# Kernel tuning notes

Hardware: AMD Instinct MI355X
Metric: run time of the kernel (lower is better)

## Reference

```python
import jax, jax.numpy as jnp
import numpy as np

M = 41
RHO = 4.0
HDIM = 10
NMODES = 2
BATCH = 16384


def triplet_index(m_size, rho):
    # reduced PBC triplet index set: n >= m, |m|,|n|,|m+n| <= (M-1)/2, |m*n| <= rho*(M-1)/2
    h = (m_size - 1) // 2
    idx = [(m, n) for m in range(-h, h + 1) for n in range(m, h + 1)
           if abs(m + n) <= h and abs(m * n) <= rho * h]
    return np.array(idx, dtype=np.int32)

IDX = triplet_index(M, RHO)
S = len(IDX)


def _c(a):
    # last-dim-2 real tensor -> complex
    return jax.lax.complex(a[..., 0], a[..., 1])


def setup_inputs() -> dict:
    key = jax.random.key(0)
    ks = jax.random.split(key, 6)
    x = jax.random.normal(ks[0], (BATCH, M, NMODES, 2), dtype=jnp.float32)
    task_info = jax.random.uniform(ks[1], (BATCH, 4), dtype=jnp.float32)  # col 0 = power in dBm
    pbc_C = 0.01 * jax.random.normal(ks[2], (S, 2), dtype=jnp.float32)  # complex PBC coeffs
    W1 = jax.random.normal(ks[3], (HDIM, NMODES, S, 2), dtype=jnp.float32) / np.sqrt(2.0 * NMODES * S)
    b1 = jnp.zeros((HDIM, 2), dtype=jnp.float32)
    W2 = jax.random.normal(ks[4], (HDIM, NMODES, M, 2), dtype=jnp.float32) / np.sqrt(2.0 * NMODES * M)
    b2 = jnp.zeros((HDIM, 2), dtype=jnp.float32)
    m_idx = jnp.asarray(IDX[:, 0], dtype=jnp.int32)
    n_idx = jnp.asarray(IDX[:, 1], dtype=jnp.int32)
    return {"x": x, "task_info": task_info, "pbc_C": pbc_C,
            "W1": W1, "b1": b1, "W2": W2, "b2": b2,
            "m_idx": m_idx, "n_idx": n_idx}


def _nonlinear_features(E, m_idx, n_idx):
    # E: [B, M, 2] complex -> [B, 2, S]; Manakov dual-pol triplets:
    # F[p] = (E[c+m,p]*conj(E[c+m+n,p]) + E[c+m,q]*conj(E[c+m+n,q])) * E[c+n,p]
    c = E.shape[1] // 2
    A = E[:, c + m_idx, :] * jnp.conj(E[:, c + m_idx + n_idx, :])  # [B, S, 2]
    F = (A + A[..., ::-1]) * E[:, c + n_idx, :]                    # [B, S, 2]
    return jnp.transpose(F, (0, 2, 1))                             # [B, 2, S]


def _conv_full(Wc, bc, inp):
    # ComplexConv1d whose kernel spans the whole input length (output length 1) -> [B, out]
    return jnp.einsum('oik,bik->bo', Wc, inp) + bc


def _forward(x, task_info, pbc_C, W1, b1, W2, b2, m_idx, n_idx):
    E = _c(x)                                    # [B, M, 2] complex64
    c = M // 2
    P = 10.0 ** (task_info[:, 0] / 10.0) / NMODES  # [B] launch power per mode
    F = _nonlinear_features(E, m_idx, n_idx)     # [B, 2, S]
    # EqAMPBC: center symbol + P * (triplet features . complex coeffs)
    pbc_out = E[:, c, :] + P[:, None] * jnp.einsum('bps,s->bp', F, _c(pbc_C))  # [B, 2]
    w1, bb1, w2, bb2 = _c(W1), _c(b1), _c(W2), _c(b2)
    # A = cat([f1(fo), f1(fo with pols flipped)], dim=-1) -> [B, hdim, 2]
    A = jnp.stack([_conv_full(w1, bb1, F), _conv_full(w1, bb1, F[:, ::-1, :])], axis=-1)
    Et = jnp.transpose(E, (0, 2, 1))             # [B, 2, M]
    Bm = jnp.stack([_conv_full(w2, bb2, Et), _conv_full(w2, bb2, Et[:, ::-1, :])], axis=-1)
    term = jnp.sum(A * Bm * jnp.conj(Bm) + jnp.conj(A) * Bm * Bm, axis=1)  # [B, 2]
    out = pbc_out + (1e-4 / np.sqrt(HDIM)) * term * (P[:, None] ** 2)
    return jnp.stack([out.real, out.imag], axis=-1)  # [B, 2, 2] float32


def reference(x, task_info, pbc_C, W1, b1, W2, b2, m_idx, n_idx):
    return _forward(x, task_info, pbc_C, W1, b1, W2, b2, m_idx, n_idx)
```

## Files before the change

### kernel.cpp

```cpp
#include <hip/hip_runtime.h>
#include <hip/hip_bf16.h>

typedef short bf16x8 __attribute__((ext_vector_type(8)));
typedef float f32x4  __attribute__((ext_vector_type(4)));

#define ROWS  96
#define KS1   56
#define KS2   6
#define NCOL  32

#define WP_OFF   0
#define W2P_OFF  344064

#define E_OFF    0
#define MET_OFF  10496
#define LDS_BYTES 22528

__device__ __forceinline__ unsigned short f2bf(float f) {
    union { float f; unsigned u; } v; v.f = f;
    unsigned r = v.u + 0x7FFFu + ((v.u >> 16) & 1u);
    return (unsigned short)(r >> 16);
}
__device__ __forceinline__ float bfl(unsigned u) {
    union { unsigned q; float f; } v; v.q = u << 16; return v.f;
}
__device__ __forceinline__ float bfh(unsigned u) {
    union { unsigned q; float f; } v; v.q = u & 0xffff0000u; return v.f;
}
__device__ __forceinline__ unsigned pk2(float a, float b) {
    __hip_bfloat162 h = __float22bfloat162_rn(make_float2(a, b));
    unsigned u; __builtin_memcpy(&u, &h, 4); return u;
}
__device__ __forceinline__ bf16x8 asbf(uint4 v) {
    union { uint4 u; bf16x8 b; } z; z.u = v; return z.b;
}

__global__ void prep_kernel(const float* __restrict__ W1,
                            const float* __restrict__ W2,
                            const float* __restrict__ pbcC,
                            unsigned short* __restrict__ Wp,
                            unsigned short* __restrict__ W2p, int S) {
    int idx = blockIdx.x * 256 + threadIdx.x;
    const int N1 = KS1 * ROWS * 8, N2 = KS2 * ROWS * 8;
    if (idx < N1) {
        int ks = idx / (ROWS * 8), rem = idx - ks * (ROWS * 8);
        int row = rem >> 3, kq = rem & 7;
        int s = ks * 8 + kq;
        float2 wj0 = make_float2(0.f, 0.f), wj1 = make_float2(0.f, 0.f);
        int p = 0, r = 0;
        if (s < S) {
            if (row < 80) {
                int o = row >> 2; p = (row >> 1) & 1; r = row & 1;
                wj0 = ((const float2*)W1)[(size_t)(o * 2 + 0) * S + s];
                wj1 = ((const float2*)W1)[(size_t)(o * 2 + 1) * S + s];
            } else if (row < 84) {
                p = (row >> 1) & 1; r = row & 1;
                wj0 = ((const float2*)pbcC)[s];
            }
        }
        ushort4 h; unsigned short us[4];
#pragma unroll
        for (int t = 0; t < 4; ++t) {
            int i = t & 1, cc = t >> 1, j = i ^ p;
            float2 w = j ? wj1 : wj0;
            float v = (cc == 0) ? (r ? w.y : w.x) : (r ? w.x : -w.y);
            us[t] = f2bf(v);
        }
        h.x = us[0]; h.y = us[1]; h.z = us[2]; h.w = us[3];
        ((ushort4*)Wp)[(size_t)(ks * ROWS + row) * 8 + kq] = h;
        return;
    }
    idx -= N1;
    if (idx < N2) {
        int ks = idx / (ROWS * 8), rem = idx - ks * (ROWS * 8);
        int row = rem >> 3, kq = rem & 7;
        int m = ks * 8 + kq;
        float2 wj0 = make_float2(0.f, 0.f), wj1 = make_float2(0.f, 0.f);
        int p = 0, r = 0;
        if (m < 41 && row < 80) {
            int o = row >> 2; p = (row >> 1) & 1; r = row & 1;
            wj0 = ((const float2*)W2)[(o * 2 + 0) * 41 + m];
            wj1 = ((const float2*)W2)[(o * 2 + 1) * 41 + m];
        }
        ushort4 h; unsigned short us[4];
#pragma unroll
        for (int t = 0; t < 4; ++t) {
            int i = t & 1, cc = t >> 1, j = i ^ p;
            float2 w = j ? wj1 : wj0;
            float v = (cc == 0) ? (r ? w.y : w.x) : (r ? w.x : -w.y);
            us[t] = f2bf(v);
        }
        h.x = us[0]; h.y = us[1]; h.z = us[2]; h.w = us[3];
        ((ushort4*)W2p)[(size_t)(ks * ROWS + row) * 8 + kq] = h;
    }
}

__global__ __launch_bounds__(256, 2) void eqsonn_kernel(
    const float* __restrict__ x,
    const float* __restrict__ task,
    const unsigned short* __restrict__ Wp,
    const unsigned short* __restrict__ W2p,
    const int* __restrict__ m_idx, const int* __restrict__ n_idx,
    const float* __restrict__ b1, const float* __restrict__ b2,
    float* __restrict__ out, int B, int S)
{
    __shared__ alignas(16) char ldsb[LDS_BYTES];
    const int tid  = threadIdx.x;
    const int lane = tid & 63;
    const int kh   = __builtin_amdgcn_readfirstlane(tid >> 6);
    const int l15  = lane & 15;
    const int quad = lane >> 4;
    const int b0   = blockIdx.x * NCOL;

    for (int e = tid; e < 41 * NCOL; e += 256) {
        int bb = e / 41, k = e - bb * 41;
        int bs = b0 + bb; if (bs > B - 1) bs = B - 1;
        float4 v = ((const float4*)x)[(size_t)bs * 41 + k];
        ushort4 h;
        h.x = f2bf(v.x); h.y = f2bf(v.y); h.z = f2bf(v.z); h.w = f2bf(v.w);
        *(ushort4*)(ldsb + E_OFF + (k * 16 + (bb & 15)) * 16 + (bb >> 4) * 8) = h;
    }
    for (int i = tid; i < 448; i += 256) {
        int2 mm = (i < S) ? make_int2(m_idx[i], n_idx[i]) : make_int2(0, 0);
        *(int2*)(ldsb + MET_OFF + i * 8) = mm;
    }
    __syncthreads();

    f32x4 a1[6][2], a2[5][2];
#pragma unroll
    for (int i = 0; i < 6; ++i) a1[i][0] = a1[i][1] = (f32x4){0.f,0.f,0.f,0.f};
#pragma unroll
    for (int i = 0; i < 5; ++i) a2[i][0] = a2[i][1] = (f32x4){0.f,0.f,0.f,0.f};

    const unsigned short* apb = Wp + l15 * 32 + quad * 8;

    for (int ks = kh * 14; ks < kh * 14 + 14; ++ks) {
        bf16x8 Af[6];
        const unsigned short* ap = apb + ks * (96 * 32);
#pragma unroll
        for (int mt = 0; mt < 6; ++mt) Af[mt] = *(const bf16x8*)(ap + mt * 512);

        unsigned g0[4], g1[4];
        int sb = ks * 8 + quad * 2;
#pragma unroll
        for (int j = 0; j < 2; ++j) {
            int2 mm = *(const int2*)(ldsb + MET_OFF + (sb + j) * 8);
            uint4 um = *(const uint4*)(ldsb + E_OFF + ((20 + mm.x) * 16 + l15) * 16);
            uint4 ub = *(const uint4*)(ldsb + E_OFF + ((20 + mm.x + mm.y) * 16 + l15) * 16);
            uint4 un = *(const uint4*)(ldsb + E_OFF + ((20 + mm.y) * 16 + l15) * 16);
#pragma unroll
            for (int g = 0; g < 2; ++g) {
                unsigned umx = g ? um.z : um.x, umy = g ? um.w : um.y;
                unsigned ubx = g ? ub.z : ub.x, uby = g ? ub.w : ub.y;
                unsigned unx = g ? un.z : un.x, uny = g ? un.w : un.y;
                float Em0r = bfl(umx), Em0i = bfh(umx), Em1r = bfl(umy), Em1i = bfh(umy);
                float Eb0r = bfl(ubx), Eb0i = bfh(ubx), Eb1r = bfl(uby), Eb1i = bfh(uby);
                float En0r = bfl(unx), En0i = bfh(unx), En1r = bfl(uny), En1i = bfh(uny);
                float sr = Em0r * Eb0r + Em0i * Eb0i + Em1r * Eb1r + Em1i * Eb1i;
                float si = Em0i * Eb0r - Em0r * Eb0i + Em1i * Eb1r - Em1r * Eb1i;
                float F0r = sr * En0r - si * En0i, F0i = sr * En0i + si * En0r;
                float F1r = sr * En1r - si * En1i, F1i = sr * En1i + si * En1r;
                unsigned* gg = g ? g1 : g0;
                gg[j * 2 + 0] = pk2(F0r, F1r);
                gg[j * 2 + 1] = pk2(F0i, F1i);
            }
        }
        bf16x8 bf0 = asbf(make_uint4(g0[0], g0[1], g0[2], g0[3]));
        bf16x8 bf1 = asbf(make_uint4(g1[0], g1[1], g1[2], g1[3]));
#pragma unroll
        for (int mt = 0; mt < 6; ++mt) {
            a1[mt][0] = __builtin_amdgcn_mfma_f32_16x16x32_bf16(Af[mt], bf0, a1[mt][0], 0, 0, 0);
            a1[mt][1] = __builtin_amdgcn_mfma_f32_16x16x32_bf16(Af[mt], bf1, a1[mt][1], 0, 0, 0);
        }
    }

    for (int k2 = kh; k2 < 6; k2 += 4) {
        bf16x8 Af[5];
        const unsigned short* ap = W2p + k2 * (96 * 32) + l15 * 32 + quad * 8;
#pragma unroll
        for (int mt = 0; mt < 5; ++mt) Af[mt] = *(const bf16x8*)(ap + mt * 512);
        unsigned g0[4], g1[4];
        int mb = k2 * 8 + quad * 2;
#pragma unroll
        for (int j = 0; j < 2; ++j) {
            int m = mb + j;
            int mc = m < 41 ? m : 40;
            uint4 ue = *(const uint4*)(ldsb + E_OFF + (mc * 16 + l15) * 16);
            bool ok = (m < 41);
            unsigned lo0 = ok ? ((ue.x & 0xffffu) | (ue.y << 16)) : 0u;
            unsigned hi0 = ok ? ((ue.x >> 16) | (ue.y & 0xffff0000u)) : 0u;
            unsigned lo1 = ok ? ((ue.z & 0xffffu) | (ue.w << 16)) : 0u;
            unsigned hi1 = ok ? ((ue.z >> 16) | (ue.w & 0xffff0000u)) : 0u;
            g0[j * 2] = lo0; g0[j * 2 + 1] = hi0;
            g1[j * 2] = lo1; g1[j * 2 + 1] = hi1;
        }
        bf16x8 bf0 = asbf(make_uint4(g0[0], g0[1], g0[2], g0[3]));
        bf16x8 bf1 = asbf(make_uint4(g1[0], g1[1], g1[2], g1[3]));
#pragma unroll
        for (int mt = 0; mt < 5; ++mt) {
            a2[mt][0] = __builtin_amdgcn_mfma_f32_16x16x32_bf16(Af[mt], bf0, a2[mt][0], 0, 0, 0);
            a2[mt][1] = __builtin_amdgcn_mfma_f32_16x16x32_bf16(Af[mt], bf1, a2[mt][1], 0, 0, 0);
        }
    }

    __syncthreads();
    float* Sum = (float*)ldsb;
#pragma unroll
    for (int ph = 0; ph < 4; ++ph) {
        if (kh == ph) {
#pragma unroll
            for (int mt = 0; mt < 6; ++mt)
#pragma unroll
                for (int g = 0; g < 2; ++g)
#pragma unroll
                    for (int reg = 0; reg < 4; ++reg) {
                        int rc = (mt * 16 + quad * 4 + reg) * 32 + g * 16 + l15;
                        if (ph == 0) Sum[rc] = a1[mt][g][reg]; else Sum[rc] += a1[mt][g][reg];
                    }
#pragma unroll
            for (int mt = 0; mt < 5; ++mt)
#pragma unroll
                for (int g = 0; g < 2; ++g)
#pragma unroll
                    for (int reg = 0; reg < 4; ++reg) {
                        int rc = (96 + mt * 16 + quad * 4 + reg) * 32 + g * 16 + l15;
                        if (ph == 0) Sum[rc] = a2[mt][g][reg]; else Sum[rc] += a2[mt][g][reg];
                    }
        }
        __syncthreads();
    }

    if (kh == 0 && lane < NCOL) {
        int col = lane;
        float pr0 = Sum[80 * 32 + col], pi0 = Sum[81 * 32 + col];
        float pr1 = Sum[82 * 32 + col], pi1 = Sum[83 * 32 + col];
        float t0 = 0.f, t1 = 0.f, t2 = 0.f, t3 = 0.f;
#pragma unroll
        for (int o = 0; o < 10; ++o) {
            float b2r = b2[o * 2], b2i = b2[o * 2 + 1];
            float b1r = b1[o * 2], b1i = b1[o * 2 + 1];
            int rb = o * 4;
            float B0r = Sum[(96 + rb + 0) * 32 + col] + b2r;
            float B0i = Sum[(96 + rb + 1) * 32 + col] + b2i;
            float B1r = Sum[(96 + rb + 2) * 32 + col] + b2r;
            float B1i = Sum[(96 + rb + 3) * 32 + col] + b2i;
            float A0r = Sum[(rb + 0) * 32 + col] + b1r;
            float A0i = Sum[(rb + 1) * 32 + col] + b1i;
            float A1r = Sum[(rb + 2) * 32 + col] + b1r;
            float A1i = Sum[(rb + 3) * 32 + col] + b1i;
            float g0 = 2.f * (A0r * B0r + A0i * B0i);
            t0 += g0 * B0r; t1 += g0 * B0i;
            float g1 = 2.f * (A1r * B1r + A1i * B1i);
            t2 += g1 * B1r; t3 += g1 * B1i;
        }
        int b = b0 + col;
        if (b < B) {
            float dbm = task[(size_t)b * 4];
            float P   = exp2f(dbm * 0.33219280948873623f) * 0.5f;
            float kP2 = 3.1622776601683794e-05f * P * P;
            float4 Ec = ((const float4*)x)[(size_t)b * 41 + 20];
            float4 o4;
            o4.x = Ec.x + P * pr0 + kP2 * t0;
            o4.y = Ec.y + P * pi0 + kP2 * t1;
            o4.z = Ec.z + P * pr1 + kP2 * t2;
            o4.w = Ec.w + P * pi1 + kP2 * t3;
            ((float4*)out)[b] = o4;
        }
    }
}

extern "C" void kernel_launch(void* const* d_in, const int* in_sizes, int n_in,
                              void* d_out, int out_size, void* d_ws, size_t ws_size,
                              hipStream_t stream) {
    const float* x     = (const float*)d_in[0];
    const float* task  = (const float*)d_in[1];
    const float* pbcC  = (const float*)d_in[2];
    const float* W1    = (const float*)d_in[3];
    const float* b1    = (const float*)d_in[4];
    const float* W2    = (const float*)d_in[5];
    const float* b2    = (const float*)d_in[6];
    const int*   m_idx = (const int*)d_in[7];
    const int*   n_idx = (const int*)d_in[8];
    float* out = (float*)d_out;

    int S = in_sizes[7];
    int B = in_sizes[0] / (41 * 2 * 2);

    char* ws = (char*)d_ws;
    unsigned short* Wp  = (unsigned short*)(ws + WP_OFF);
    unsigned short* W2p = (unsigned short*)(ws + W2P_OFF);

    int prep_n = KS1 * ROWS * 8 + KS2 * ROWS * 8;
    prep_kernel<<<(prep_n + 255) / 256, 256, 0, stream>>>(W1, W2, pbcC, Wp, W2p, S);

    int grid = (B + NCOL - 1) / NCOL;
    eqsonn_kernel<<<grid, 256, 0, stream>>>(x, task, Wp, W2p, m_idx, n_idx,
                                            b1, b2, out, B, S);
}
```

Before: 99.48 us.

## Switch to 32x32x16 MFMA with lane-major weight layout and pipelined feature gather

Replaces the 16x16x32 bf16 MFMA tiling with 32x32x16 MFMA. The weights are repacked in the prep kernel into a per-lane contiguous layout, so each A fragment is a single coalesced load. E is stored per column with a padded stride, and the triplet metadata is precomputed as LDS byte offsets. Triplet feature loads are software-pipelined one k-step ahead. Occupancy is raised to 3 blocks per SM, with separate LDS for the reduction sums. The aim is fewer MFMA issues, less LDS index arithmetic and better latency hiding, at the cost of more LDS per block and a two-stage reduction.

```diff
diff --git a/kernel.cpp b/kernel.cpp
--- a/kernel.cpp
+++ b/kernel.cpp
@@ -2,19 +2,19 @@
 #include <hip/hip_bf16.h>
 
 typedef short bf16x8 __attribute__((ext_vector_type(8)));
-typedef float f32x4  __attribute__((ext_vector_type(4)));
-
-#define ROWS  96
-#define KS1   56
-#define KS2   6
+typedef float f32x16 __attribute__((ext_vector_type(16)));
+
 #define NCOL  32
+#define KS1   112
+#define KS2   12
+#define ESTR  264
 
 #define WP_OFF   0
 #define W2P_OFF  344064
 
-#define E_OFF    0
-#define MET_OFF  10496
-#define LDS_BYTES 22528
+#define MET_OFF  10824
+#define SUM_OFF  14544
+#define LDS_BYTES 39120
 
 __device__ __forceinline__ unsigned short f2bf(float f) {
     union { float f; unsigned u; } v; v.f = f;
@@ -33,6 +33,12 @@
 }
 __device__ __forceinline__ bf16x8 asbf(uint4 v) {
     union { uint4 u; bf16x8 b; } z; z.u = v; return z.b;
+}
+__device__ __forceinline__ f32x16 zero16() {
+    f32x16 z;
+#pragma unroll
+    for (int i = 0; i < 16; ++i) z[i] = 0.f;
+    return z;
 }
 
 __global__ void prep_kernel(const float* __restrict__ W1,
@@ -41,11 +47,15 @@
                             unsigned short* __restrict__ Wp,
                             unsigned short* __restrict__ W2p, int S) {
     int idx = blockIdx.x * 256 + threadIdx.x;
-    const int N1 = KS1 * ROWS * 8, N2 = KS2 * ROWS * 8;
+    const int N1 = KS1 * 3 * 64 * 2;
+    const int N2 = KS2 * 3 * 64 * 2;
     if (idx < N1) {
-        int ks = idx / (ROWS * 8), rem = idx - ks * (ROWS * 8);
-        int row = rem >> 3, kq = rem & 7;
-        int s = ks * 8 + kq;
+        int ks = idx / 384, rem = idx - ks * 384;
+        int mt = rem >> 7; rem &= 127;
+        int lane = rem >> 1, jh = rem & 1;
+        int row = mt * 32 + (lane & 31);
+        int kg  = ks * 16 + (lane >> 5) * 8 + jh * 4;
+        int s   = kg >> 2;
         float2 wj0 = make_float2(0.f, 0.f), wj1 = make_float2(0.f, 0.f);
         int p = 0, r = 0;
         if (s < S) {
@@ -61,20 +71,23 @@
         ushort4 h; unsigned short us[4];
 #pragma unroll
         for (int t = 0; t < 4; ++t) {
-            int i = t & 1, cc = t >> 1, j = i ^ p;
-            float2 w = j ? wj1 : wj0;
+            int i = t & 1, cc = t >> 1, j2 = i ^ p;
+            float2 w = j2 ? wj1 : wj0;
             float v = (cc == 0) ? (r ? w.y : w.x) : (r ? w.x : -w.y);
             us[t] = f2bf(v);
         }
         h.x = us[0]; h.y = us[1]; h.z = us[2]; h.w = us[3];
-        ((ushort4*)Wp)[(size_t)(ks * ROWS + row) * 8 + kq] = h;
+        ((ushort4*)Wp)[idx] = h;
         return;
     }
     idx -= N1;
     if (idx < N2) {
-        int ks = idx / (ROWS * 8), rem = idx - ks * (ROWS * 8);
-        int row = rem >> 3, kq = rem & 7;
-        int m = ks * 8 + kq;
+        int ks = idx / 384, rem = idx - ks * 384;
+        int mt = rem >> 7; rem &= 127;
+        int lane = rem >> 1, jh = rem & 1;
+        int row = mt * 32 + (lane & 31);
+        int kg  = ks * 16 + (lane >> 5) * 8 + jh * 4;
+        int m   = kg >> 2;
         float2 wj0 = make_float2(0.f, 0.f), wj1 = make_float2(0.f, 0.f);
         int p = 0, r = 0;
         if (m < 41 && row < 80) {
@@ -85,19 +98,18 @@
         ushort4 h; unsigned short us[4];
 #pragma unroll
         for (int t = 0; t < 4; ++t) {
-            int i = t & 1, cc = t >> 1, j = i ^ p;
-            float2 w = j ? wj1 : wj0;
+            int i = t & 1, cc = t >> 1, j2 = i ^ p;
+            float2 w = j2 ? wj1 : wj0;
             float v = (cc == 0) ? (r ? w.y : w.x) : (r ? w.x : -w.y);
             us[t] = f2bf(v);
         }
         h.x = us[0]; h.y = us[1]; h.z = us[2]; h.w = us[3];
-        ((ushort4*)W2p)[(size_t)(ks * ROWS + row) * 8 + kq] = h;
-    }
-}
-
-__global__ __launch_bounds__(256, 2) void eqsonn_kernel(
-    const float* __restrict__ x,
-    const float* __restrict__ task,
+        ((ushort4*)W2p)[idx] = h;
+    }
+}
+
+__global__ __launch_bounds__(256, 3) void eqsonn_kernel(
+    const float* __restrict__ x, const float* __restrict__ task,
     const unsigned short* __restrict__ Wp,
     const unsigned short* __restrict__ W2p,
     const int* __restrict__ m_idx, const int* __restrict__ n_idx,
@@ -107,9 +119,9 @@
     __shared__ alignas(16) char ldsb[LDS_BYTES];
     const int tid  = threadIdx.x;
     const int lane = tid & 63;
-    const int kh   = __builtin_amdgcn_readfirstlane(tid >> 6);
-    const int l15  = lane & 15;
-    const int quad = lane >> 4;
+    const int w    = __builtin_amdgcn_readfirstlane(tid >> 6);
+    const int col  = lane & 31;
+    const int kha  = lane >> 5;
     const int b0   = blockIdx.x * NCOL;
 
     for (int e = tid; e < 41 * NCOL; e += 256) {
@@ -118,142 +130,140 @@
         float4 v = ((const float4*)x)[(size_t)bs * 41 + k];
         ushort4 h;
         h.x = f2bf(v.x); h.y = f2bf(v.y); h.z = f2bf(v.z); h.w = f2bf(v.w);
-        *(ushort4*)(ldsb + E_OFF + (k * 16 + (bb & 15)) * 16 + (bb >> 4) * 8) = h;
-    }
-    for (int i = tid; i < 448; i += 256) {
-        int2 mm = (i < S) ? make_int2(m_idx[i], n_idx[i]) : make_int2(0, 0);
-        *(int2*)(ldsb + MET_OFF + i * 8) = mm;
+        *(ushort4*)(ldsb + k * ESTR + bb * 8) = h;
+    }
+    for (int i = tid; i < 464; i += 256) {
+        int m = 0, n = 0;
+        if (i < S) { m = m_idx[i]; n = n_idx[i]; }
+        unsigned offM = (unsigned)((20 + m) * ESTR);
+        unsigned offB = (unsigned)((20 + m + n) * ESTR);
+        unsigned offN = (unsigned)((20 + n) * ESTR);
+        *(uint2*)(ldsb + MET_OFF + i * 8) = make_uint2(offM | (offB << 16), offN);
     }
     __syncthreads();
 
-    f32x4 a1[6][2], a2[5][2];
-#pragma unroll
-    for (int i = 0; i < 6; ++i) a1[i][0] = a1[i][1] = (f32x4){0.f,0.f,0.f,0.f};
-#pragma unroll
-    for (int i = 0; i < 5; ++i) a2[i][0] = a2[i][1] = (f32x4){0.f,0.f,0.f,0.f};
-
-    const unsigned short* apb = Wp + l15 * 32 + quad * 8;
-
-    for (int ks = kh * 14; ks < kh * 14 + 14; ++ks) {
-        bf16x8 Af[6];
-        const unsigned short* ap = apb + ks * (96 * 32);
-#pragma unroll
-        for (int mt = 0; mt < 6; ++mt) Af[mt] = *(const bf16x8*)(ap + mt * 512);
-
-        unsigned g0[4], g1[4];
-        int sb = ks * 8 + quad * 2;
-#pragma unroll
-        for (int j = 0; j < 2; ++j) {
-            int2 mm = *(const int2*)(ldsb + MET_OFF + (sb + j) * 8);
-            uint4 um = *(const uint4*)(ldsb + E_OFF + ((20 + mm.x) * 16 + l15) * 16);
-            uint4 ub = *(const uint4*)(ldsb + E_OFF + ((20 + mm.x + mm.y) * 16 + l15) * 16);
-            uint4 un = *(const uint4*)(ldsb + E_OFF + ((20 + mm.y) * 16 + l15) * 16);
-#pragma unroll
-            for (int g = 0; g < 2; ++g) {
-                unsigned umx = g ? um.z : um.x, umy = g ? um.w : um.y;
-                unsigned ubx = g ? ub.z : ub.x, uby = g ? ub.w : ub.y;
-                unsigned unx = g ? un.z : un.x, uny = g ? un.w : un.y;
-                float Em0r = bfl(umx), Em0i = bfh(umx), Em1r = bfl(umy), Em1i = bfh(umy);
-                float Eb0r = bfl(ubx), Eb0i = bfh(ubx), Eb1r = bfl(uby), Eb1i = bfh(uby);
-                float En0r = bfl(unx), En0i = bfh(unx), En1r = bfl(uny), En1i = bfh(uny);
-                float sr = Em0r * Eb0r + Em0i * Eb0i + Em1r * Eb1r + Em1i * Eb1i;
-                float si = Em0i * Eb0r - Em0r * Eb0i + Em1i * Eb1r - Em1r * Eb1i;
-                float F0r = sr * En0r - si * En0i, F0i = sr * En0i + si * En0r;
-                float F1r = sr * En1r - si * En1i, F1i = sr * En1i + si * En1r;
-                unsigned* gg = g ? g1 : g0;
-                gg[j * 2 + 0] = pk2(F0r, F1r);
-                gg[j * 2 + 1] = pk2(F0i, F1i);
+    const char* Ebase = ldsb + col * 8;
+    auto ldM4 = [&](int ks) -> uint4 {
+        return *(const uint4*)(ldsb + MET_OFF + (ks * 4 + kha * 2) * 8);
+    };
+    auto ldE = [&](unsigned off) -> uint2 {
+        return *(const uint2*)(Ebase + off);
+    };
+    auto fbuild = [&](uint2 em, uint2 eq, uint2 en, unsigned& lo, unsigned& hi) {
+        float m0r = bfl(em.x), m0i = bfh(em.x), m1r = bfl(em.y), m1i = bfh(em.y);
+        float q0r = bfl(eq.x), q0i = bfh(eq.x), q1r = bfl(eq.y), q1i = bfh(eq.y);
+        float n0r = bfl(en.x), n0i = bfh(en.x), n1r = bfl(en.y), n1i = bfh(en.y);
+        float sr = m0r * q0r + m0i * q0i + m1r * q1r + m1i * q1i;
+        float si = m0i * q0r - m0r * q0i + m1i * q1r - m1r * q1i;
+        float F0r = sr * n0r - si * n0i, F0i = sr * n0i + si * n0r;
+        float F1r = sr * n1r - si * n1i, F1i = sr * n1i + si * n1r;
+        lo = pk2(F0r, F1r); hi = pk2(F0i, F1i);
+    };
+
+    f32x16 ac0 = zero16(), ac1 = zero16(), ac2 = zero16();
+    {
+        const int ks0 = w * 28;
+        uint4 M = ldM4(ks0);
+        uint2 e0 = ldE(M.x & 0xffffu), e1 = ldE(M.x >> 16), e2 = ldE(M.y);
+        uint2 e3 = ldE(M.z & 0xffffu), e4 = ldE(M.z >> 16), e5 = ldE(M.w);
+        uint4 Mc = ldM4(ks0 + 1);
+        const short* Wp16 = (const short*)Wp;
+        for (int ks = ks0; ks < ks0 + 28; ++ks) {
+            const short* ap = Wp16 + (size_t)ks * 1536 + lane * 8;
+            bf16x8 A0 = *(const bf16x8*)(ap);
+            bf16x8 A1 = *(const bf16x8*)(ap + 512);
+            bf16x8 A2 = *(const bf16x8*)(ap + 1024);
+            uint2 f0 = ldE(Mc.x & 0xffffu), f1v = ldE(Mc.x >> 16), f2v = ldE(Mc.y);
+            uint2 f3 = ldE(Mc.z & 0xffffu), f4v = ldE(Mc.z >> 16), f5v = ldE(Mc.w);
+            uint4 Mn = ldM4(ks + 2);
+            unsigned g0, g1, g2, g3;
+            fbuild(e0, e1, e2, g0, g1);
+            fbuild(e3, e4, e5, g2, g3);
+            bf16x8 bfr = asbf(make_uint4(g0, g1, g2, g3));
+            ac0 = __builtin_amdgcn_mfma_f32_32x32x16_bf16(A0, bfr, ac0, 0, 0, 0);
+            ac1 = __builtin_amdgcn_mfma_f32_32x32x16_bf16(A1, bfr, ac1, 0, 0, 0);
+            ac2 = __builtin_amdgcn_mfma_f32_32x32x16_bf16(A2, bfr, ac2, 0, 0, 0);
+            e0 = f0; e1 = f1v; e2 = f2v; e3 = f3; e4 = f4v; e5 = f5v; Mc = Mn;
+        }
+    }
+
+    __syncthreads();
+    float* Sum = (float*)(ldsb + SUM_OFF);
+    auto dump = [&](f32x16 a, int baserow, bool add) {
+#pragma unroll
+        for (int reg = 0; reg < 16; ++reg) {
+            int row = baserow + (reg & 3) + 8 * (reg >> 2) + 4 * kha;
+            int idx = row * 32 + col;
+            if (add) Sum[idx] += a[reg]; else Sum[idx] = a[reg];
+        }
+    };
+    for (int ph = 0; ph < 4; ++ph) {
+        if (w == ph) {
+            bool add = (ph != 0);
+            dump(ac0, 0, add); dump(ac1, 32, add); dump(ac2, 64, add);
+        }
+        __syncthreads();
+    }
+
+    f32x16 bc0 = zero16(), bc1 = zero16(), bc2 = zero16();
+    {
+        const short* W216 = (const short*)W2p;
+        for (int t = 0; t < 3; ++t) {
+            int ks2 = w * 3 + t;
+            const short* ap = W216 + (size_t)ks2 * 1536 + lane * 8;
+            bf16x8 A0 = *(const bf16x8*)(ap);
+            bf16x8 A1 = *(const bf16x8*)(ap + 512);
+            bf16x8 A2 = *(const bf16x8*)(ap + 1024);
+            unsigned g[4];
+#pragma unroll
+            for (int j = 0; j < 2; ++j) {
+                int m = ks2 * 4 + kha * 2 + j;
+                int mc = m < 41 ? m : 40;
+                uint2 ue = *(const uint2*)(ldsb + mc * ESTR + col * 8);
+                unsigned lo = (ue.x & 0xffffu) | (ue.y << 16);
+                unsigned hi = (ue.x >> 16) | (ue.y & 0xffff0000u);
+                if (m >= 41) { lo = 0u; hi = 0u; }
+                g[j * 2] = lo; g[j * 2 + 1] = hi;
             }
-        }
-        bf16x8 bf0 = asbf(make_uint4(g0[0], g0[1], g0[2], g0[3]));
-        bf16x8 bf1 = asbf(make_uint4(g1[0], g1[1], g1[2], g1[3]));
-#pragma unroll
-        for (int mt = 0; mt < 6; ++mt) {
-            a1[mt][0] = __builtin_amdgcn_mfma_f32_16x16x32_bf16(Af[mt], bf0, a1[mt][0], 0, 0, 0);
-            a1[mt][1] = __builtin_amdgcn_mfma_f32_16x16x32_bf16(Af[mt], bf1, a1[mt][1], 0, 0, 0);
-        }
-    }
-
-    for (int k2 = kh; k2 < 6; k2 += 4) {
-        bf16x8 Af[5];
-        const unsigned short* ap = W2p + k2 * (96 * 32) + l15 * 32 + quad * 8;
-#pragma unroll
-        for (int mt = 0; mt < 5; ++mt) Af[mt] = *(const bf16x8*)(ap + mt * 512);
-        unsigned g0[4], g1[4];
-        int mb = k2 * 8 + quad * 2;
-#pragma unroll
-        for (int j = 0; j < 2; ++j) {
-            int m = mb + j;
-            int mc = m < 41 ? m : 40;
-            uint4 ue = *(const uint4*)(ldsb + E_OFF + (mc * 16 + l15) * 16);
-            bool ok = (m < 41);
-            unsigned lo0 = ok ? ((ue.x & 0xffffu) | (ue.y << 16)) : 0u;
-            unsigned hi0 = ok ? ((ue.x >> 16) | (ue.y & 0xffff0000u)) : 0u;
-            unsigned lo1 = ok ? ((ue.z & 0xffffu) | (ue.w << 16)) : 0u;
-            unsigned hi1 = ok ? ((ue.z >> 16) | (ue.w & 0xffff0000u)) : 0u;
-            g0[j * 2] = lo0; g0[j * 2 + 1] = hi0;
-            g1[j * 2] = lo1; g1[j * 2 + 1] = hi1;
-        }
-        bf16x8 bf0 = asbf(make_uint4(g0[0], g0[1], g0[2], g0[3]));
-        bf16x8 bf1 = asbf(make_uint4(g1[0], g1[1], g1[2], g1[3]));
-#pragma unroll
-        for (int mt = 0; mt < 5; ++mt) {
-            a2[mt][0] = __builtin_amdgcn_mfma_f32_16x16x32_bf16(Af[mt], bf0, a2[mt][0], 0, 0, 0);
-            a2[mt][1] = __builtin_amdgcn_mfma_f32_16x16x32_bf16(Af[mt], bf1, a2[mt][1], 0, 0, 0);
-        }
-    }
-
+            bf16x8 bfr = asbf(make_uint4(g[0], g[1], g[2], g[3]));
+            bc0 = __builtin_amdgcn_mfma_f32_32x32x16_bf16(A0, bfr, bc0, 0, 0, 0);
+            bc1 = __builtin_amdgcn_mfma_f32_32x32x16_bf16(A1, bfr, bc1, 0, 0, 0);
+            bc2 = __builtin_amdgcn_mfma_f32_32x32x16_bf16(A2, bfr, bc2, 0, 0, 0);
+        }
+    }
     __syncthreads();
-    float* Sum = (float*)ldsb;
-#pragma unroll
     for (int ph = 0; ph < 4; ++ph) {
-        if (kh == ph) {
-#pragma unroll
-            for (int mt = 0; mt < 6; ++mt)
-#pragma unroll
-                for (int g = 0; g < 2; ++g)
-#pragma unroll
-                    for (int reg = 0; reg < 4; ++reg) {
-                        int rc = (mt * 16 + quad * 4 + reg) * 32 + g * 16 + l15;
-                        if (ph == 0) Sum[rc] = a1[mt][g][reg]; else Sum[rc] += a1[mt][g][reg];
-                    }
-#pragma unroll
-            for (int mt = 0; mt < 5; ++mt)
-#pragma unroll
-                for (int g = 0; g < 2; ++g)
-#pragma unroll
-                    for (int reg = 0; reg < 4; ++reg) {
-                        int rc = (96 + mt * 16 + quad * 4 + reg) * 32 + g * 16 + l15;
-                        if (ph == 0) Sum[rc] = a2[mt][g][reg]; else Sum[rc] += a2[mt][g][reg];
-                    }
+        if (w == ph) {
+            bool add = (ph != 0);
+            dump(bc0, 96, add); dump(bc1, 128, add); dump(bc2, 160, add);
         }
         __syncthreads();
     }
 
-    if (kh == 0 && lane < NCOL) {
-        int col = lane;
-        float pr0 = Sum[80 * 32 + col], pi0 = Sum[81 * 32 + col];
-        float pr1 = Sum[82 * 32 + col], pi1 = Sum[83 * 32 + col];
+    if (w == 0 && lane < NCOL) {
+        int c = lane;
+        float pr0 = Sum[80 * 32 + c], pi0 = Sum[81 * 32 + c];
+        float pr1 = Sum[82 * 32 + c], pi1 = Sum[83 * 32 + c];
         float t0 = 0.f, t1 = 0.f, t2 = 0.f, t3 = 0.f;
 #pragma unroll
         for (int o = 0; o < 10; ++o) {
             float b2r = b2[o * 2], b2i = b2[o * 2 + 1];
             float b1r = b1[o * 2], b1i = b1[o * 2 + 1];
             int rb = o * 4;
-            float B0r = Sum[(96 + rb + 0) * 32 + col] + b2r;
-            float B0i = Sum[(96 + rb + 1) * 32 + col] + b2i;
-            float B1r = Sum[(96 + rb + 2) * 32 + col] + b2r;
-            float B1i = Sum[(96 + rb + 3) * 32 + col] + b2i;
-            float A0r = Sum[(rb + 0) * 32 + col] + b1r;
-            float A0i = Sum[(rb + 1) * 32 + col] + b1i;
-            float A1r = Sum[(rb + 2) * 32 + col] + b1r;
-            float A1i = Sum[(rb + 3) * 32 + col] + b1i;
+            float B0r = Sum[(96 + rb + 0) * 32 + c] + b2r;
+            float B0i = Sum[(96 + rb + 1) * 32 + c] + b2i;
+            float B1r = Sum[(96 + rb + 2) * 32 + c] + b2r;
+            float B1i = Sum[(96 + rb + 3) * 32 + c] + b2i;
+            float A0r = Sum[(rb + 0) * 32 + c] + b1r;
+            float A0i = Sum[(rb + 1) * 32 + c] + b1i;
+            float A1r = Sum[(rb + 2) * 32 + c] + b1r;
+            float A1i = Sum[(rb + 3) * 32 + c] + b1i;
             float g0 = 2.f * (A0r * B0r + A0i * B0i);
             t0 += g0 * B0r; t1 += g0 * B0i;
             float g1 = 2.f * (A1r * B1r + A1i * B1i);
             t2 += g1 * B1r; t3 += g1 * B1i;
         }
-        int b = b0 + col;
+        int b = b0 + c;
         if (b < B) {
             float dbm = task[(size_t)b * 4];
             float P   = exp2f(dbm * 0.33219280948873623f) * 0.5f;
@@ -290,7 +300,7 @@
     unsigned short* Wp  = (unsigned short*)(ws + WP_OFF);
     unsigned short* W2p = (unsigned short*)(ws + W2P_OFF);
 
-    int prep_n = KS1 * ROWS * 8 + KS2 * ROWS * 8;
+    int prep_n = KS1 * 3 * 64 * 2 + KS2 * 3 * 64 * 2;
     prep_kernel<<<(prep_n + 255) / 256, 256, 0, stream>>>(W1, W2, pbcC, Wp, W2p, S);
 
     int grid = (B + NCOL - 1) / NCOL;
```

Result: slower. 101.7 us (+2.3%).
